# Kernel tuning notes

Hardware: AMD Instinct MI355X
Metric: run time of the kernel (lower is better)

Reference implementation:

```python
import jax, jax.numpy as jnp
import numpy as np

C, K, D = 64, 512, 2048   # classes, shots per class, hidden_dim
N_ITER = 3                # n_routing_iter


def _squash(x):
    # x: (..., d); squash along last axis: x * ||x|| / (1 + ||x||^2)
    n2 = jnp.sum(x * x, axis=-1, keepdims=True)
    n = jnp.sqrt(n2)
    return x * (n / (1.0 + n2))


def setup_inputs() -> dict:
    key = jax.random.key(0)
    z_s = jax.random.normal(key, (C, K, D), dtype=jnp.float32)
    return {"z_s": z_s}


def reference(z_s):
    # z_s: (C, K, D). All C classes routed in parallel (vectorized over the
    # original Python loop over classes).
    z_sq = _squash(z_s)                       # (C, K, D)
    b = jnp.zeros(z_s.shape[:2], z_s.dtype)   # routing logits (C, K)
    c = jnp.zeros((z_s.shape[0], z_s.shape[2]), z_s.dtype)
    for _ in range(N_ITER):
        d = jax.nn.softmax(b, axis=-1)                      # (C, K)
        c = _squash(jnp.einsum('ck,ckd->cd', d, z_sq))      # (C, D)
        b = b + jnp.einsum('ckd,cd->ck', z_sq, c)           # (C, K)
    # returned representative is c from the LAST iteration (b update after is unused,
    # matching the torch loop where c_i from the final iter is appended)
    return c
```

## Files before the change

### kernel.cpp

```cpp
#include <hip/hip_runtime.h>
#include <math.h>

#define C_CLS  64
#define K_SHOTS 512
#define D_DIM  2048
#define BPC    16
#define ROWS_PER_BLOCK (K_SHOTS / BPC)
#define NWAVES 4
#define ROWS_PER_WAVE (ROWS_PER_BLOCK / NWAVES)
#define NBLK   (C_CLS * BPC)
#define NF4    8

__device__ __forceinline__ float wave_reduce_sum(float v) {
#pragma unroll
    for (int off = 32; off > 0; off >>= 1)
        v += __shfl_xor(v, off, 64);
    return v;
}

template <int PASS>
__global__ __launch_bounds__(256)
void route_pass(const float* __restrict__ z,
                float* __restrict__ scale,
                float* __restrict__ bvec,
                const float* __restrict__ c_prev,
                float* __restrict__ part_s,
                float* __restrict__ part_e)
{
    __shared__ float4 s_comb[NWAVES][D_DIM / 4];
    __shared__ float  e_comb[NWAVES];

    const int blk  = blockIdx.x;
    const int cls  = blk / BPC;
    const int bic  = blk - cls * BPC;
    const int lane = threadIdx.x & 63;
    const int wid  = threadIdx.x >> 6;

    float4 cp[NF4];
    if (PASS != 0) {
        const float4* cp4 = (const float4*)(c_prev + (size_t)cls * D_DIM);
#pragma unroll
        for (int i = 0; i < NF4; ++i) cp[i] = cp4[lane + i * 64];
    }

    float4 acc[NF4];
#pragma unroll
    for (int i = 0; i < NF4; ++i) acc[i] = make_float4(0.f, 0.f, 0.f, 0.f);
    float esum = 0.f;

    const int k0 = bic * ROWS_PER_BLOCK + wid * ROWS_PER_WAVE;
    const float4* __restrict__ zbase =
        (const float4*)(z + ((size_t)cls * K_SHOTS + k0) * D_DIM);

    float4 zcur[NF4];
#pragma unroll
    for (int i = 0; i < NF4; ++i) zcur[i] = zbase[lane + i * 64];

#pragma unroll
    for (int r = 0; r < ROWS_PER_WAVE; ++r) {
        float4 znext[NF4];
        if (r + 1 < ROWS_PER_WAVE) {
            const float4* zn = zbase + (size_t)(r + 1) * (D_DIM / 4);
#pragma unroll
            for (int i = 0; i < NF4; ++i) znext[i] = zn[lane + i * 64];
        }
        const int k = k0 + r;
        float w, sc;
        if (PASS == 0) {
            float n2 = 0.f;
#pragma unroll
            for (int i = 0; i < NF4; ++i) {
                n2 += zcur[i].x * zcur[i].x + zcur[i].y * zcur[i].y
                    + zcur[i].z * zcur[i].z + zcur[i].w * zcur[i].w;
            }
            n2 = wave_reduce_sum(n2);
            sc = sqrtf(n2) / (1.f + n2);
            if (lane == 0) scale[cls * K_SHOTS + k] = sc;
            w = 1.f;
        } else {
            float dot = 0.f;
#pragma unroll
            for (int i = 0; i < NF4; ++i) {
                dot += zcur[i].x * cp[i].x + zcur[i].y * cp[i].y
                     + zcur[i].z * cp[i].z + zcur[i].w * cp[i].w;
            }
            dot = wave_reduce_sum(dot);
            sc = scale[cls * K_SHOTS + k];
            float bnew = sc * dot;
            if (PASS == 2) bnew += bvec[cls * K_SHOTS + k];
            if (lane == 0) bvec[cls * K_SHOTS + k] = bnew;
            w = expf(bnew);
        }
        esum += w;
        const float wsc = w * sc;
#pragma unroll
        for (int i = 0; i < NF4; ++i) {
            acc[i].x += wsc * zcur[i].x;
            acc[i].y += wsc * zcur[i].y;
            acc[i].z += wsc * zcur[i].z;
            acc[i].w += wsc * zcur[i].w;
        }
        if (r + 1 < ROWS_PER_WAVE) {
#pragma unroll
            for (int i = 0; i < NF4; ++i) zcur[i] = znext[i];
        }
    }

#pragma unroll
    for (int i = 0; i < NF4; ++i) s_comb[wid][lane + i * 64] = acc[i];
    if (lane == 0) e_comb[wid] = esum;
    __syncthreads();

    float4* ps = (float4*)(part_s + (size_t)blk * D_DIM);
    const int t = threadIdx.x;
#pragma unroll
    for (int j = 0; j < 2; ++j) {
        const int f = t + j * 256;
        const float4 a = s_comb[0][f];
        const float4 b4 = s_comb[1][f];
        const float4 c4 = s_comb[2][f];
        const float4 d4 = s_comb[3][f];
        float4 s;
        s.x = (a.x + b4.x) + (c4.x + d4.x);
        s.y = (a.y + b4.y) + (c4.y + d4.y);
        s.z = (a.z + b4.z) + (c4.z + d4.z);
        s.w = (a.w + b4.w) + (c4.w + d4.w);
        ps[f] = s;
    }
    if (t == 0) part_e[blk] = (e_comb[0] + e_comb[1]) + (e_comb[2] + e_comb[3]);
}

__global__ __launch_bounds__(256)
void reduce_squash(const float* __restrict__ part_s,
                   const float* __restrict__ part_e,
                   float* __restrict__ c_out)
{
    __shared__ float wred[NWAVES];
    const int cls  = blockIdx.x;
    const int t    = threadIdx.x;
    const int lane = t & 63;
    const int wid  = t >> 6;

    float esum = 0.f;
#pragma unroll
    for (int p = 0; p < BPC; ++p) esum += part_e[cls * BPC + p];
    const float inv = 1.f / esum;

    float4 m[2];
    float n2p = 0.f;
#pragma unroll
    for (int j = 0; j < 2; ++j) {
        const int f = t + j * 256;
        float4 s = make_float4(0.f, 0.f, 0.f, 0.f);
        for (int p = 0; p < BPC; ++p) {
            const float4 v =
                ((const float4*)(part_s + (size_t)(cls * BPC + p) * D_DIM))[f];
            s.x += v.x; s.y += v.y; s.z += v.z; s.w += v.w;
        }
        m[j].x = s.x * inv; m[j].y = s.y * inv;
        m[j].z = s.z * inv; m[j].w = s.w * inv;
        n2p += m[j].x * m[j].x + m[j].y * m[j].y
             + m[j].z * m[j].z + m[j].w * m[j].w;
    }
    float n2 = wave_reduce_sum(n2p);
    if (lane == 0) wred[wid] = n2;
    __syncthreads();
    n2 = (wred[0] + wred[1]) + (wred[2] + wred[3]);
    const float fac = sqrtf(n2) / (1.f + n2);

    float4* co = (float4*)(c_out + (size_t)cls * D_DIM);
#pragma unroll
    for (int j = 0; j < 2; ++j) {
        const int f = t + j * 256;
        float4 o;
        o.x = m[j].x * fac; o.y = m[j].y * fac;
        o.z = m[j].z * fac; o.w = m[j].w * fac;
        co[f] = o;
    }
}

extern "C" void kernel_launch(void* const* d_in, const int* in_sizes, int n_in,
                              void* d_out, int out_size, void* d_ws, size_t ws_size,
                              hipStream_t stream)
{
    const float* z = (const float*)d_in[0];
    float* out = (float*)d_out;
    float* ws  = (float*)d_ws;

    float* scale  = ws;
    float* bvec   = scale + C_CLS * K_SHOTS;
    float* c_buf  = bvec + C_CLS * K_SHOTS;
    float* part_s = c_buf + (size_t)C_CLS * D_DIM;
    float* part_e = part_s + (size_t)NBLK * D_DIM;

    route_pass<0><<<NBLK, 256, 0, stream>>>(z, scale, bvec, nullptr, part_s, part_e);
    reduce_squash<<<C_CLS, 256, 0, stream>>>(part_s, part_e, c_buf);

    route_pass<1><<<NBLK, 256, 0, stream>>>(z, scale, bvec, c_buf, part_s, part_e);
    reduce_squash<<<C_CLS, 256, 0, stream>>>(part_s, part_e, c_buf);

    route_pass<2><<<NBLK, 256, 0, stream>>>(z, scale, bvec, c_buf, part_s, part_e);
    reduce_squash<<<C_CLS, 256, 0, stream>>>(part_s, part_e, out);
}
```

Baseline: 151.0 us.

## Fuse per-class reduce-squash into route pass via last-block atomic ticket

Drops the separate reduce_squash kernels: each route block takes an atomic ticket per class, and the last block for a class reduces the partials and writes the squashed class vector. This removes three kernel launches and their gaps, at the cost of a memset and atomics. It also reverses the block order in pass 1 to reuse z rows still in cache from pass 0, drops the explicit register double-buffering in favour of a non-unrolled loop, and sets an occupancy hint in the launch bounds. The risk is reduced latency hiding without the software prefetch.

```diff
diff --git a/kernel.cpp b/kernel.cpp
--- a/kernel.cpp
+++ b/kernel.cpp
@@ -1,15 +1,15 @@
 #include <hip/hip_runtime.h>
 #include <math.h>
 
-#define C_CLS  64
+#define C_CLS   64
 #define K_SHOTS 512
-#define D_DIM  2048
-#define BPC    16
+#define D_DIM   2048
+#define BPC     16
 #define ROWS_PER_BLOCK (K_SHOTS / BPC)
-#define NWAVES 4
+#define NWAVES  4
 #define ROWS_PER_WAVE (ROWS_PER_BLOCK / NWAVES)
-#define NBLK   (C_CLS * BPC)
-#define NF4    8
+#define NBLK    (C_CLS * BPC)
+#define NF4     8
 
 __device__ __forceinline__ float wave_reduce_sum(float v) {
 #pragma unroll
@@ -19,22 +19,27 @@
 }
 
 template <int PASS>
-__global__ __launch_bounds__(256)
+__global__ __launch_bounds__(256, 4)
 void route_pass(const float* __restrict__ z,
                 float* __restrict__ scale,
                 float* __restrict__ bvec,
                 const float* __restrict__ c_prev,
+                float* __restrict__ c_out,
                 float* __restrict__ part_s,
-                float* __restrict__ part_e)
+                float* __restrict__ part_e,
+                unsigned int* __restrict__ cnt)
 {
     __shared__ float4 s_comb[NWAVES][D_DIM / 4];
     __shared__ float  e_comb[NWAVES];
+    __shared__ unsigned int s_ticket;
 
-    const int blk  = blockIdx.x;
-    const int cls  = blk / BPC;
-    const int bic  = blk - cls * BPC;
+    const int rawblk = blockIdx.x;
+    const int blk  = (PASS == 1) ? (NBLK - 1 - rawblk) : rawblk;
+    const int cls  = blk >> 4;
+    const int bic  = blk & (BPC - 1);
     const int lane = threadIdx.x & 63;
     const int wid  = threadIdx.x >> 6;
+    const int t    = threadIdx.x;
 
     float4 cp[NF4];
     if (PASS != 0) {
@@ -52,27 +57,21 @@
     const float4* __restrict__ zbase =
         (const float4*)(z + ((size_t)cls * K_SHOTS + k0) * D_DIM);
 
-    float4 zcur[NF4];
+#pragma unroll 1
+    for (int r = 0; r < ROWS_PER_WAVE; ++r) {
+        const float4* zr = zbase + (size_t)r * (D_DIM / 4);
+        float4 zc[NF4];
 #pragma unroll
-    for (int i = 0; i < NF4; ++i) zcur[i] = zbase[lane + i * 64];
+        for (int i = 0; i < NF4; ++i) zc[i] = zr[lane + i * 64];
 
-#pragma unroll
-    for (int r = 0; r < ROWS_PER_WAVE; ++r) {
-        float4 znext[NF4];
-        if (r + 1 < ROWS_PER_WAVE) {
-            const float4* zn = zbase + (size_t)(r + 1) * (D_DIM / 4);
-#pragma unroll
-            for (int i = 0; i < NF4; ++i) znext[i] = zn[lane + i * 64];
-        }
         const int k = k0 + r;
         float w, sc;
         if (PASS == 0) {
             float n2 = 0.f;
 #pragma unroll
-            for (int i = 0; i < NF4; ++i) {
-                n2 += zcur[i].x * zcur[i].x + zcur[i].y * zcur[i].y
-                    + zcur[i].z * zcur[i].z + zcur[i].w * zcur[i].w;
-            }
+            for (int i = 0; i < NF4; ++i)
+                n2 += zc[i].x * zc[i].x + zc[i].y * zc[i].y
+                    + zc[i].z * zc[i].z + zc[i].w * zc[i].w;
             n2 = wave_reduce_sum(n2);
             sc = sqrtf(n2) / (1.f + n2);
             if (lane == 0) scale[cls * K_SHOTS + k] = sc;
@@ -80,29 +79,24 @@
         } else {
             float dot = 0.f;
 #pragma unroll
-            for (int i = 0; i < NF4; ++i) {
-                dot += zcur[i].x * cp[i].x + zcur[i].y * cp[i].y
-                     + zcur[i].z * cp[i].z + zcur[i].w * cp[i].w;
-            }
+            for (int i = 0; i < NF4; ++i)
+                dot += zc[i].x * cp[i].x + zc[i].y * cp[i].y
+                     + zc[i].z * cp[i].z + zc[i].w * cp[i].w;
             dot = wave_reduce_sum(dot);
             sc = scale[cls * K_SHOTS + k];
             float bnew = sc * dot;
             if (PASS == 2) bnew += bvec[cls * K_SHOTS + k];
-            if (lane == 0) bvec[cls * K_SHOTS + k] = bnew;
+            if (PASS == 1 && lane == 0) bvec[cls * K_SHOTS + k] = bnew;
             w = expf(bnew);
         }
         esum += w;
         const float wsc = w * sc;
 #pragma unroll
         for (int i = 0; i < NF4; ++i) {
-            acc[i].x += wsc * zcur[i].x;
-            acc[i].y += wsc * zcur[i].y;
-            acc[i].z += wsc * zcur[i].z;
-            acc[i].w += wsc * zcur[i].w;
-        }
-        if (r + 1 < ROWS_PER_WAVE) {
-#pragma unroll
-            for (int i = 0; i < NF4; ++i) zcur[i] = znext[i];
+            acc[i].x += wsc * zc[i].x;
+            acc[i].y += wsc * zc[i].y;
+            acc[i].z += wsc * zc[i].z;
+            acc[i].w += wsc * zc[i].w;
         }
     }
 
@@ -112,11 +106,10 @@
     __syncthreads();
 
     float4* ps = (float4*)(part_s + (size_t)blk * D_DIM);
-    const int t = threadIdx.x;
 #pragma unroll
     for (int j = 0; j < 2; ++j) {
         const int f = t + j * 256;
-        const float4 a = s_comb[0][f];
+        const float4 a  = s_comb[0][f];
         const float4 b4 = s_comb[1][f];
         const float4 c4 = s_comb[2][f];
         const float4 d4 = s_comb[3][f];
@@ -128,23 +121,19 @@
         ps[f] = s;
     }
     if (t == 0) part_e[blk] = (e_comb[0] + e_comb[1]) + (e_comb[2] + e_comb[3]);
-}
 
-__global__ __launch_bounds__(256)
-void reduce_squash(const float* __restrict__ part_s,
-                   const float* __restrict__ part_e,
-                   float* __restrict__ c_out)
-{
-    __shared__ float wred[NWAVES];
-    const int cls  = blockIdx.x;
-    const int t    = threadIdx.x;
-    const int lane = t & 63;
-    const int wid  = t >> 6;
+    __syncthreads();
+    if (t == 0)
+        s_ticket = __hip_atomic_fetch_add(&cnt[cls], 1u,
+                                          __ATOMIC_ACQ_REL,
+                                          __HIP_MEMORY_SCOPE_AGENT);
+    __syncthreads();
+    if (s_ticket != BPC - 1) return;
 
-    float esum = 0.f;
+    float es = 0.f;
 #pragma unroll
-    for (int p = 0; p < BPC; ++p) esum += part_e[cls * BPC + p];
-    const float inv = 1.f / esum;
+    for (int p = 0; p < BPC; ++p) es += part_e[cls * BPC + p];
+    const float inv = 1.f / es;
 
     float4 m[2];
     float n2p = 0.f;
@@ -152,6 +141,7 @@
     for (int j = 0; j < 2; ++j) {
         const int f = t + j * 256;
         float4 s = make_float4(0.f, 0.f, 0.f, 0.f);
+#pragma unroll
         for (int p = 0; p < BPC; ++p) {
             const float4 v =
                 ((const float4*)(part_s + (size_t)(cls * BPC + p) * D_DIM))[f];
@@ -163,9 +153,9 @@
              + m[j].z * m[j].z + m[j].w * m[j].w;
     }
     float n2 = wave_reduce_sum(n2p);
-    if (lane == 0) wred[wid] = n2;
+    if (lane == 0) e_comb[wid] = n2;
     __syncthreads();
-    n2 = (wred[0] + wred[1]) + (wred[2] + wred[3]);
+    n2 = (e_comb[0] + e_comb[1]) + (e_comb[2] + e_comb[3]);
     const float fac = sqrtf(n2) / (1.f + n2);
 
     float4* co = (float4*)(c_out + (size_t)cls * D_DIM);
@@ -189,16 +179,18 @@
 
     float* scale  = ws;
     float* bvec   = scale + C_CLS * K_SHOTS;
-    float* c_buf  = bvec + C_CLS * K_SHOTS;
-    float* part_s = c_buf + (size_t)C_CLS * D_DIM;
+    float* c1     = bvec + C_CLS * K_SHOTS;
+    float* c2     = c1 + (size_t)C_CLS * D_DIM;
+    float* part_s = c2 + (size_t)C_CLS * D_DIM;
     float* part_e = part_s + (size_t)NBLK * D_DIM;
+    unsigned int* cnt = (unsigned int*)(part_e + NBLK);
 
-    route_pass<0><<<NBLK, 256, 0, stream>>>(z, scale, bvec, nullptr, part_s, part_e);
-    reduce_squash<<<C_CLS, 256, 0, stream>>>(part_s, part_e, c_buf);
+    hipMemsetAsync(cnt, 0, 3 * C_CLS * sizeof(unsigned int), stream);
 
-    route_pass<1><<<NBLK, 256, 0, stream>>>(z, scale, bvec, c_buf, part_s, part_e);
-    reduce_squash<<<C_CLS, 256, 0, stream>>>(part_s, part_e, c_buf);
-
-    route_pass<2><<<NBLK, 256, 0, stream>>>(z, scale, bvec, c_buf, part_s, part_e);
-    reduce_squash<<<C_CLS, 256, 0, stream>>>(part_s, part_e, out);
+    route_pass<0><<<NBLK, 256, 0, stream>>>(z, scale, bvec, nullptr, c1,
+                                            part_s, part_e, cnt);
+    route_pass<1><<<NBLK, 256, 0, stream>>>(z, scale, bvec, c1, c2,
+                                            part_s, part_e, cnt + C_CLS);
+    route_pass<2><<<NBLK, 256, 0, stream>>>(z, scale, bvec, c2, out,
+                                            part_s, part_e, cnt + 2 * C_CLS);
 }
```

Result: slower. 282.9 us (+87.4%).
